# Optimization experiments

Measured on AMD Instinct MI355X. Metric: run time of the kernel, lower is better.

Reference implementation:

```python
import jax, jax.numpy as jnp
import numpy as np

B, L, H, NH = 2, 2048, 1024, 16
HD = H // NH  # head dim = 64


def setup_inputs() -> dict:
    key = jax.random.key(0)
    ks = jax.random.split(key, 8)
    s = 0.02  # small init scale for weights
    return {
        "q": jax.random.normal(ks[0], (B, L, H), jnp.float32),
        "k": jax.random.normal(ks[1], (B, L, H), jnp.float32),
        "v": jax.random.normal(ks[2], (B, L, H), jnp.float32),
        "attention_mask": jnp.zeros((B, NH, L, L), jnp.float32),
        "Wq": jax.random.normal(ks[3], (H, H), jnp.float32) * s,
        "bq": jnp.zeros((H,), jnp.float32),
        "Wk": jax.random.normal(ks[4], (H, H), jnp.float32) * s,
        "bk": jnp.zeros((H,), jnp.float32),
        "Wv": jax.random.normal(ks[5], (H, H), jnp.float32) * s,
        "bv": jnp.zeros((H,), jnp.float32),
        "Wo": jax.random.normal(ks[6], (H, H), jnp.float32) * s,
        "bo": jnp.zeros((H,), jnp.float32),
    }


def reference(q, k, v, attention_mask, Wq, bq, Wk, bk, Wv, bv, Wo, bo):
    # Conv1D (GPT-2 style) projections: x @ W + b
    query = q @ Wq + bq  # [B, L, H]
    key = k @ Wk + bk
    value = v @ Wv + bv
    # split heads -> [B, NH, L, HD]
    qh = query.reshape(B, L, NH, HD).transpose(0, 2, 1, 3)
    kh = key.reshape(B, L, NH, HD).transpose(0, 2, 1, 3)
    vh = value.reshape(B, L, NH, HD).transpose(0, 2, 1, 3)
    # scores: [B, NH, L, L]
    w = jnp.einsum("bhqd,bhkd->bhqk", qh, kh) / jnp.sqrt(jnp.float32(HD))
    w = w + attention_mask
    w = jax.nn.softmax(w, axis=-1)  # dropout p=0 -> identity
    out = jnp.einsum("bhqk,bhkd->bhqd", w, vh)  # [B, NH, L, HD]
    # merge heads -> [B, L, H]
    out = out.transpose(0, 2, 1, 3).reshape(B, L, H)
    return out @ Wo + bo
```

## Files before the change

kernel.cpp:

```cpp
#include <hip/hip_runtime.h>

#define NBATCH 2
#define LSEQ   2048
#define NH     16
#define HD     64
#define HDIM   1024
#define MTOK   4096

typedef unsigned short u16;
typedef __attribute__((ext_vector_type(8))) short bf16x8;
typedef __attribute__((ext_vector_type(4))) float f32x4;

__device__ __forceinline__ u16 f2bf(float f) {
  union { float f; unsigned int u; } x; x.f = f;
  return (u16)((x.u + 0x7fffu + ((x.u >> 16) & 1u)) >> 16);
}

__device__ __forceinline__ void gload_lds16(const void* g, void* l) {
  __builtin_amdgcn_global_load_lds(
      (const __attribute__((address_space(1))) unsigned int*)g,
      (__attribute__((address_space(3))) unsigned int*)l, 16, 0, 0);
}

__global__ void cvt3_kernel(const float* __restrict__ q, const float* __restrict__ k,
                            const float* __restrict__ v, u16* __restrict__ xq,
                            u16* __restrict__ xk, u16* __restrict__ xv) {
  const float* in;
  u16* out;
  if (blockIdx.z == 0)      { in = q; out = xq; }
  else if (blockIdx.z == 1) { in = k; out = xk; }
  else                      { in = v; out = xv; }
  int i = blockIdx.x * blockDim.x + threadIdx.x;
  float4 t = ((const float4*)in)[i];
  ushort4 o;
  o.x = f2bf(t.x); o.y = f2bf(t.y); o.z = f2bf(t.z); o.w = f2bf(t.w);
  ((ushort4*)out)[i] = o;
}

__global__ void wt4_kernel(const float* __restrict__ W0, const float* __restrict__ W1,
                           const float* __restrict__ W2, const float* __restrict__ W3,
                           u16* __restrict__ T0, u16* __restrict__ T1,
                           u16* __restrict__ T2, u16* __restrict__ T3) {
  const float* W;
  u16* Wt;
  if (blockIdx.z == 0)      { W = W0; Wt = T0; }
  else if (blockIdx.z == 1) { W = W1; Wt = T1; }
  else if (blockIdx.z == 2) { W = W2; Wt = T2; }
  else                      { W = W3; Wt = T3; }
  __shared__ float tile[64][65];
  const int k0 = (blockIdx.x & 15) << 6;
  const int n0 = (blockIdx.x >> 4) << 6;
  const int t = threadIdx.x;
#pragma unroll
  for (int i = 0; i < 4; ++i) {
    int idx = t + i * 256;
    int r = idx >> 4, c = (idx & 15) << 2;
    float4 v = *(const float4*)&W[(size_t)(k0 + r) * HDIM + n0 + c];
    tile[r][c] = v.x; tile[r][c + 1] = v.y; tile[r][c + 2] = v.z; tile[r][c + 3] = v.w;
  }
  __syncthreads();
#pragma unroll
  for (int i = 0; i < 4; ++i) {
    int idx = t + i * 256;
    int r = idx >> 4, c = (idx & 15) << 2;
    ushort4 o;
    o.x = f2bf(tile[c][r]);     o.y = f2bf(tile[c + 1][r]);
    o.z = f2bf(tile[c + 2][r]); o.w = f2bf(tile[c + 3][r]);
    *(ushort4*)&Wt[(size_t)(n0 + r) * HDIM + k0 + c] = o;
  }
}

template <int MODE>
__device__ __forceinline__ void gemm_core(u16* As, u16* Bs,
    const u16* __restrict__ A, const u16* __restrict__ Bt,
    const float* __restrict__ bias, void* __restrict__ Cout) {
  const int tid = threadIdx.x;
  const int lane = tid & 63, wid = tid >> 6;
  const int l15 = lane & 15, g = lane >> 4;
  const int m0 = blockIdx.y * 128, n0 = blockIdx.x * 128;
  const int wr = wid >> 1, wc = wid & 1;
  f32x4 acc[4][4];
#pragma unroll
  for (int i = 0; i < 4; ++i)
#pragma unroll
    for (int j = 0; j < 4; ++j) acc[i][j] = (f32x4){0.f, 0.f, 0.f, 0.f};

  for (int t = 0; t < HDIM / 64; ++t) {
    const int k0 = t * 64;
    __syncthreads();
#pragma unroll
    for (int i = 0; i < 4; ++i) {
      const int row = wid * 32 + i * 8 + (lane >> 3);
      const int colb = (lane & 7) * 16;
      gload_lds16((const char*)(A + (size_t)(m0 + row) * HDIM + k0) + colb,
                  (char*)As + (wid * 32 + i * 8) * 128);
      gload_lds16((const char*)(Bt + (size_t)(n0 + row) * HDIM + k0) + colb,
                  (char*)Bs + (wid * 32 + i * 8) * 128);
    }
    __syncthreads();
#pragma unroll
    for (int ks = 0; ks < 2; ++ks) {
      bf16x8 a[4], b[4];
#pragma unroll
      for (int i = 0; i < 4; ++i) {
        const int row = wr * 64 + i * 16 + l15;
        a[i] = *(const bf16x8*)((const char*)As + row * 128 + ks * 64 + g * 16);
      }
#pragma unroll
      for (int j = 0; j < 4; ++j) {
        const int row = wc * 64 + j * 16 + l15;
        b[j] = *(const bf16x8*)((const char*)Bs + row * 128 + ks * 64 + g * 16);
      }
#pragma unroll
      for (int i = 0; i < 4; ++i)
#pragma unroll
        for (int j = 0; j < 4; ++j)
          acc[i][j] = __builtin_amdgcn_mfma_f32_16x16x32_bf16(a[i], b[j], acc[i][j], 0, 0, 0);
    }
  }
#pragma unroll
  for (int i = 0; i < 4; ++i) {
    const int mrow = m0 + wr * 64 + i * 16 + 4 * g;
#pragma unroll
    for (int j = 0; j < 4; ++j) {
      const int ncol = n0 + wc * 64 + j * 16 + l15;
      const float bb = bias[ncol];
      if (MODE == 3) {
        float* o = (float*)Cout;
#pragma unroll
        for (int r = 0; r < 4; ++r)
          o[(size_t)(mrow + r) * HDIM + ncol] = acc[i][j][r] + bb;
      } else if (MODE == 2) {
        const int bidx = mrow >> 11, l0 = mrow & (LSEQ - 1);
        const int h = ncol >> 6, d = ncol & 63;
        ushort4 o4;
        o4.x = f2bf(acc[i][j][0] + bb); o4.y = f2bf(acc[i][j][1] + bb);
        o4.z = f2bf(acc[i][j][2] + bb); o4.w = f2bf(acc[i][j][3] + bb);
        *(ushort4*)&((u16*)Cout)[(((size_t)bidx * NH + h) * HD + d) * LSEQ + l0] = o4;
      } else {
        const int h = ncol >> 6, d = ncol & 63;
        u16* o = (u16*)Cout;
#pragma unroll
        for (int r = 0; r < 4; ++r) {
          const int m = mrow + r;
          const int bidx = m >> 11, l = m & (LSEQ - 1);
          o[(((size_t)bidx * NH + h) * LSEQ + l) * HD + d] = f2bf(acc[i][j][r] + bb);
        }
      }
    }
  }
}

__global__ __launch_bounds__(256, 2) void proj_gemm_kernel(
    const u16* __restrict__ xq, const u16* __restrict__ xk, const u16* __restrict__ xv,
    const u16* __restrict__ WqT, const u16* __restrict__ WkT, const u16* __restrict__ WvT,
    const float* __restrict__ bq, const float* __restrict__ bk, const float* __restrict__ bv,
    u16* __restrict__ Qh, u16* __restrict__ Kh, u16* __restrict__ Vt) {
  __shared__ u16 As[128 * 64];
  __shared__ u16 Bs[128 * 64];
  if (blockIdx.z == 0)      gemm_core<0>(As, Bs, xq, WqT, bq, Qh);
  else if (blockIdx.z == 1) gemm_core<0>(As, Bs, xk, WkT, bk, Kh);
  else                      gemm_core<2>(As, Bs, xv, WvT, bv, Vt);
}

__global__ __launch_bounds__(256, 2) void out_gemm_kernel(
    const u16* __restrict__ A, const u16* __restrict__ WoT,
    const float* __restrict__ bo, float* __restrict__ out) {
  __shared__ u16 As[128 * 64];
  __shared__ u16 Bs[128 * 64];
  gemm_core<3>(As, Bs, A, WoT, bo, out);
}

__global__ __launch_bounds__(256, 4) void attn_kernel(
    const u16* __restrict__ Qh, const u16* __restrict__ Kh,
    const u16* __restrict__ Vt, const float* __restrict__ mask,
    u16* __restrict__ Out ) {
  __shared__ u16 Ks[2][64 * 64];
  __shared__ u16 Vs[2][64 * 64];
  __shared__ u16 Ps[4][16 * 64];
  const int lane = threadIdx.x & 63, w = threadIdx.x >> 6;
  const int l15 = lane & 15, g = lane >> 4;
  const int bh = blockIdx.y;
  const int q0 = blockIdx.x * 64 + w * 16;
  const int NT = LSEQ / 64;

  bf16x8 aq[2];
  {
    const u16* qbase = Qh + ((size_t)bh * LSEQ + q0 + l15) * HD;
    aq[0] = *(const bf16x8*)(qbase + g * 8);
    aq[1] = *(const bf16x8*)(qbase + 32 + g * 8);
  }
  f32x4 o_acc[4];
#pragma unroll
  for (int db = 0; db < 4; ++db) o_acc[db] = (f32x4){0.f, 0.f, 0.f, 0.f};
  float m_run = -1e30f, l_run = 0.f;

  const size_t kbase = (size_t)bh * LSEQ * HD;
  const size_t vbase = (size_t)bh * HD * LSEQ;
  const int srow = w * 16 + (lane >> 3);
  const int scolb = (lane & 7) * 16;

#define STAGE(buf, tt) do {                                                    \
    const int kv0_ = (tt) * 64;                                                \
    _Pragma("unroll")                                                          \
    for (int i_ = 0; i_ < 2; ++i_) {                                           \
      const int row_ = srow + i_ * 8;                                          \
      const int cb_ = scolb ^ ((row_ & 7) << 4);                               \
      gload_lds16((const char*)(Kh + kbase + (size_t)(kv0_ + row_) * HD) + cb_,\
                  (char*)Ks[buf] + (w * 16 + i_ * 8) * 128);                   \
      gload_lds16((const char*)(Vt + vbase + (size_t)row_ * LSEQ + kv0_) + cb_,\
                  (char*)Vs[buf] + (w * 16 + i_ * 8) * 128);                   \
    }                                                                          \
  } while (0)

  const float* mrow = mask + ((size_t)bh * LSEQ + q0 + l15) * LSEQ;
  f32x4 mv[4];

  STAGE(0, 0);
#pragma unroll
  for (int mb = 0; mb < 4; ++mb)
    mv[mb] = *(const f32x4*)(mrow + mb * 16 + 4 * g);
  __syncthreads();

  int cur = 0;
  u16* pbase = Ps[w];
  const int srcbase = (lane & 48) | ((lane & 48) >> 2);
  const int pswz = (l15 & 7) << 4;

  for (int t = 0; t < NT; ++t) {
    if (t + 1 < NT) STAGE(cur ^ 1, t + 1);

    f32x4 s_acc[4];
#pragma unroll
    for (int mb = 0; mb < 4; ++mb) s_acc[mb] = (f32x4){0.f, 0.f, 0.f, 0.f};
    __builtin_amdgcn_s_setprio(1);
#pragma unroll
    for (int ks = 0; ks < 2; ++ks) {
#pragma unroll
      for (int mb = 0; mb < 4; ++mb) {
        const int row = mb * 16 + l15;
        bf16x8 bk = *(const bf16x8*)((const char*)Ks[cur] + row * 128 +
                                     ((ks * 64 + g * 16) ^ ((row & 7) << 4)));
        s_acc[mb] = __builtin_amdgcn_mfma_f32_16x16x32_bf16(bk, aq[ks], s_acc[mb], 0, 0, 0);
      }
    }
    __builtin_amdgcn_s_setprio(0);

    float p[4][4];
    float tmax = -1e30f;
#pragma unroll
    for (int mb = 0; mb < 4; ++mb)
#pragma unroll
      for (int r = 0; r < 4; ++r) {
        p[mb][r] = s_acc[mb][r] * 0.125f + mv[mb][r];
        tmax = fmaxf(tmax, p[mb][r]);
      }
    tmax = fmaxf(tmax, __shfl_xor(tmax, 16));
    tmax = fmaxf(tmax, __shfl_xor(tmax, 32));
    const float mnew = fmaxf(m_run, tmax);
    const float cf = __expf(m_run - mnew);
    m_run = mnew;
    float psum = 0.f;
#pragma unroll
    for (int mb = 0; mb < 4; ++mb)
#pragma unroll
      for (int r = 0; r < 4; ++r) {
        p[mb][r] = __expf(p[mb][r] - mnew);
        psum += p[mb][r];
      }
    psum += __shfl_xor(psum, 16);
    psum += __shfl_xor(psum, 32);
    l_run = l_run * cf + psum;
    float cfr[4];
#pragma unroll
    for (int r = 0; r < 4; ++r) cfr[r] = __shfl(cf, srcbase + r);
#pragma unroll
    for (int db = 0; db < 4; ++db)
#pragma unroll
      for (int r = 0; r < 4; ++r) o_acc[db][r] *= cfr[r];

#pragma unroll
    for (int mb = 0; mb < 4; ++mb) {
      ushort4 pk;
      pk.x = f2bf(p[mb][0]); pk.y = f2bf(p[mb][1]);
      pk.z = f2bf(p[mb][2]); pk.w = f2bf(p[mb][3]);
      *(ushort4*)((char*)pbase + l15 * 128 + ((mb * 32 + 8 * g) ^ pswz)) = pk;
    }

    {
      const int tn = (t + 1 < NT) ? t + 1 : t;
      const float* mnext = mrow + tn * 64;
#pragma unroll
      for (int mb = 0; mb < 4; ++mb)
        mv[mb] = *(const f32x4*)(mnext + mb * 16 + 4 * g);
    }

    asm volatile("s_waitcnt lgkmcnt(0)" ::: "memory");
    __builtin_amdgcn_sched_barrier(0);

    __builtin_amdgcn_s_setprio(1);
#pragma unroll
    for (int s = 0; s < 2; ++s) {
      bf16x8 pa = *(const bf16x8*)((const char*)pbase + l15 * 128 +
                                   ((s * 64 + 16 * g) ^ pswz));
#pragma unroll
      for (int db = 0; db < 4; ++db) {
        const int row = db * 16 + l15;
        bf16x8 bv = *(const bf16x8*)((const char*)Vs[cur] + row * 128 +
                                     ((s * 64 + 16 * g) ^ ((row & 7) << 4)));
        o_acc[db] = __builtin_amdgcn_mfma_f32_16x16x32_bf16(pa, bv, o_acc[db], 0, 0, 0);
      }
    }
    __builtin_amdgcn_s_setprio(0);
    __syncthreads();
    cur ^= 1;
  }
#undef STAGE

  const int b = bh >> 4, h = bh & 15;
  float lr[4];
#pragma unroll
  for (int r = 0; r < 4; ++r) lr[r] = __shfl(l_run, srcbase + r);
#pragma unroll
  for (int r = 0; r < 4; ++r) {
    const float inv = 1.f / lr[r];
    const int qg = q0 + 4 * g + r;
    u16* orow = Out + ((size_t)(b * LSEQ + qg) * NH + h) * HD;
#pragma unroll
    for (int db = 0; db < 4; ++db)
      orow[db * 16 + l15] = f2bf(o_acc[db][r] * inv);
  }
}

extern "C" void kernel_launch(void* const* d_in, const int* in_sizes, int n_in,
                              void* d_out, int out_size, void* d_ws, size_t ws_size,
                              hipStream_t stream) {
  (void)in_sizes; (void)n_in; (void)out_size; (void)ws_size;
  const float* q    = (const float*)d_in[0];
  const float* k    = (const float*)d_in[1];
  const float* v    = (const float*)d_in[2];
  const float* mask = (const float*)d_in[3];
  const float* Wq   = (const float*)d_in[4];
  const float* bq   = (const float*)d_in[5];
  const float* Wk   = (const float*)d_in[6];
  const float* bk   = (const float*)d_in[7];
  const float* Wv   = (const float*)d_in[8];
  const float* bv   = (const float*)d_in[9];
  const float* Wo   = (const float*)d_in[10];
  const float* bo   = (const float*)d_in[11];
  float* out = (float*)d_out;

  char* ws = (char*)d_ws;
  const size_t XB = (size_t)MTOK * HDIM * 2;
  const size_t WB = (size_t)HDIM * HDIM * 2;
  u16* xq   = (u16*)(ws);
  u16* xk   = (u16*)(ws + XB);
  u16* xv   = (u16*)(ws + 2 * XB);
  u16* WqT  = (u16*)(ws + 3 * XB);
  u16* WkT  = (u16*)(ws + 3 * XB + WB);
  u16* WvT  = (u16*)(ws + 3 * XB + 2 * WB);
  u16* WoT  = (u16*)(ws + 3 * XB + 3 * WB);
  u16* Qh   = (u16*)(ws + 3 * XB + 4 * WB);
  u16* Kh   = (u16*)(ws + 4 * XB + 4 * WB);
  u16* Vt   = (u16*)(ws + 5 * XB + 4 * WB);
  u16* aout = (u16*)(ws + 6 * XB + 4 * WB);

  cvt3_kernel<<<dim3((MTOK * HDIM) / 4 / 256, 1, 3), 256, 0, stream>>>(
      q, k, v, xq, xk, xv);
  wt4_kernel<<<dim3(256, 1, 4), 256, 0, stream>>>(
      Wq, Wk, Wv, Wo, WqT, WkT, WvT, WoT);
  proj_gemm_kernel<<<dim3(HDIM / 128, MTOK / 128, 3), 256, 0, stream>>>(
      xq, xk, xv, WqT, WkT, WvT, bq, bk, bv, Qh, Kh, Vt);
  attn_kernel<<<dim3(LSEQ / 64, NBATCH * NH), 256, 0, stream>>>(Qh, Kh, Vt, mask, aout);
  out_gemm_kernel<<<dim3(HDIM / 128, MTOK / 128), 256, 0, stream>>>(aout, WoT, bo, out);
}
```

Before: 232.8 us.

## Stage mask via LDS, lazy softmax rescale, fuse prep kernels, remap GEMM blocks

The attention kernel now loads the mask tiles asynchronously into double-buffered LDS alongside K/V, replacing per-lane direct global loads. It also skips the online-softmax rescale when the new max exceeds the running max by at most 8, which removes the exp and the o_acc multiplies on most iterations. The two prep kernels are merged into one launch, and the GEMM grids are flattened with an XCD-aware block remap. Occupancy hints change as well: GEMMs go to 3 waves per EU and attention to 2. The extra mask LDS lowers attention occupancy, and the lazy rescale assumes exp values stay within a bounded range.

```diff
diff --git a/kernel.cpp b/kernel.cpp
--- a/kernel.cpp
+++ b/kernel.cpp
@@ -22,41 +22,37 @@
       (__attribute__((address_space(3))) unsigned int*)l, 16, 0, 0);
 }
 
-__global__ void cvt3_kernel(const float* __restrict__ q, const float* __restrict__ k,
-                            const float* __restrict__ v, u16* __restrict__ xq,
-                            u16* __restrict__ xk, u16* __restrict__ xv) {
-  const float* in;
-  u16* out;
-  if (blockIdx.z == 0)      { in = q; out = xq; }
-  else if (blockIdx.z == 1) { in = k; out = xk; }
-  else                      { in = v; out = xv; }
-  int i = blockIdx.x * blockDim.x + threadIdx.x;
-  float4 t = ((const float4*)in)[i];
-  ushort4 o;
-  o.x = f2bf(t.x); o.y = f2bf(t.y); o.z = f2bf(t.z); o.w = f2bf(t.w);
-  ((ushort4*)out)[i] = o;
-}
-
-__global__ void wt4_kernel(const float* __restrict__ W0, const float* __restrict__ W1,
-                           const float* __restrict__ W2, const float* __restrict__ W3,
-                           u16* __restrict__ T0, u16* __restrict__ T1,
-                           u16* __restrict__ T2, u16* __restrict__ T3) {
-  const float* W;
-  u16* Wt;
-  if (blockIdx.z == 0)      { W = W0; Wt = T0; }
-  else if (blockIdx.z == 1) { W = W1; Wt = T1; }
-  else if (blockIdx.z == 2) { W = W2; Wt = T2; }
-  else                      { W = W3; Wt = T3; }
+__global__ void prep_kernel(
+    const float* __restrict__ q, const float* __restrict__ k, const float* __restrict__ v,
+    const float* __restrict__ W0, const float* __restrict__ W1,
+    const float* __restrict__ W2, const float* __restrict__ W3,
+    u16* __restrict__ xq, u16* __restrict__ xk, u16* __restrict__ xv,
+    u16* __restrict__ T0, u16* __restrict__ T1, u16* __restrict__ T2,
+    u16* __restrict__ T3) {
   __shared__ float tile[64][65];
-  const int k0 = (blockIdx.x & 15) << 6;
-  const int n0 = (blockIdx.x >> 4) << 6;
+  if (blockIdx.z < 3) {
+    const float* in = (blockIdx.z == 0) ? q : (blockIdx.z == 1) ? k : v;
+    u16* out = (blockIdx.z == 0) ? xq : (blockIdx.z == 1) ? xk : xv;
+    int i = blockIdx.x * blockDim.x + threadIdx.x;
+    float4 t4 = ((const float4*)in)[i];
+    ushort4 o;
+    o.x = f2bf(t4.x); o.y = f2bf(t4.y); o.z = f2bf(t4.z); o.w = f2bf(t4.w);
+    ((ushort4*)out)[i] = o;
+    return;
+  }
+  if (blockIdx.x >= 1024) return;
+  const int sel = blockIdx.x >> 8, bx = blockIdx.x & 255;
+  const float* W = (sel == 0) ? W0 : (sel == 1) ? W1 : (sel == 2) ? W2 : W3;
+  u16* Wt = (sel == 0) ? T0 : (sel == 1) ? T1 : (sel == 2) ? T2 : T3;
+  const int k0 = (bx & 15) << 6;
+  const int n0 = (bx >> 4) << 6;
   const int t = threadIdx.x;
 #pragma unroll
   for (int i = 0; i < 4; ++i) {
     int idx = t + i * 256;
     int r = idx >> 4, c = (idx & 15) << 2;
-    float4 v = *(const float4*)&W[(size_t)(k0 + r) * HDIM + n0 + c];
-    tile[r][c] = v.x; tile[r][c + 1] = v.y; tile[r][c + 2] = v.z; tile[r][c + 3] = v.w;
+    float4 v4 = *(const float4*)&W[(size_t)(k0 + r) * HDIM + n0 + c];
+    tile[r][c] = v4.x; tile[r][c + 1] = v4.y; tile[r][c + 2] = v4.z; tile[r][c + 3] = v4.w;
   }
   __syncthreads();
 #pragma unroll
@@ -71,13 +67,12 @@
 }
 
 template <int MODE>
-__device__ __forceinline__ void gemm_core(u16* As, u16* Bs,
+__device__ __forceinline__ void gemm_core(u16* As, u16* Bs, int m0, int n0,
     const u16* __restrict__ A, const u16* __restrict__ Bt,
     const float* __restrict__ bias, void* __restrict__ Cout) {
   const int tid = threadIdx.x;
   const int lane = tid & 63, wid = tid >> 6;
   const int l15 = lane & 15, g = lane >> 4;
-  const int m0 = blockIdx.y * 128, n0 = blockIdx.x * 128;
   const int wr = wid >> 1, wc = wid & 1;
   f32x4 acc[4][4];
 #pragma unroll
@@ -151,32 +146,40 @@
   }
 }
 
-__global__ __launch_bounds__(256, 2) void proj_gemm_kernel(
+__global__ __launch_bounds__(256, 3) void proj_gemm_kernel(
     const u16* __restrict__ xq, const u16* __restrict__ xk, const u16* __restrict__ xv,
     const u16* __restrict__ WqT, const u16* __restrict__ WkT, const u16* __restrict__ WvT,
     const float* __restrict__ bq, const float* __restrict__ bk, const float* __restrict__ bv,
     u16* __restrict__ Qh, u16* __restrict__ Kh, u16* __restrict__ Vt) {
   __shared__ u16 As[128 * 64];
   __shared__ u16 Bs[128 * 64];
-  if (blockIdx.z == 0)      gemm_core<0>(As, Bs, xq, WqT, bq, Qh);
-  else if (blockIdx.z == 1) gemm_core<0>(As, Bs, xk, WkT, bk, Kh);
-  else                      gemm_core<2>(As, Bs, xv, WvT, bv, Vt);
-}
-
-__global__ __launch_bounds__(256, 2) void out_gemm_kernel(
+  const int h = blockIdx.x;
+  const int l = (h & 7) * 96 + (h >> 3);
+  const int z = l >> 8, rem = l & 255;
+  const int m0 = (rem >> 3) * 128, n0 = (rem & 7) * 128;
+  if (z == 0)      gemm_core<0>(As, Bs, m0, n0, xq, WqT, bq, Qh);
+  else if (z == 1) gemm_core<0>(As, Bs, m0, n0, xk, WkT, bk, Kh);
+  else             gemm_core<2>(As, Bs, m0, n0, xv, WvT, bv, Vt);
+}
+
+__global__ __launch_bounds__(256, 3) void out_gemm_kernel(
     const u16* __restrict__ A, const u16* __restrict__ WoT,
     const float* __restrict__ bo, float* __restrict__ out) {
   __shared__ u16 As[128 * 64];
   __shared__ u16 Bs[128 * 64];
-  gemm_core<3>(As, Bs, A, WoT, bo, out);
-}
-
-__global__ __launch_bounds__(256, 4) void attn_kernel(
+  const int h = blockIdx.x;
+  const int l = (h & 7) * 32 + (h >> 3);
+  const int m0 = (l >> 3) * 128, n0 = (l & 7) * 128;
+  gemm_core<3>(As, Bs, m0, n0, A, WoT, bo, out);
+}
+
+__global__ __launch_bounds__(256, 2) void attn_kernel(
     const u16* __restrict__ Qh, const u16* __restrict__ Kh,
     const u16* __restrict__ Vt, const float* __restrict__ mask,
     u16* __restrict__ Out ) {
   __shared__ u16 Ks[2][64 * 64];
   __shared__ u16 Vs[2][64 * 64];
+  __shared__ float Msh[2][4][16 * 64];
   __shared__ u16 Ps[4][16 * 64];
   const int lane = threadIdx.x & 63, w = threadIdx.x >> 6;
   const int l15 = lane & 15, g = lane >> 4;
@@ -199,8 +202,10 @@
   const size_t vbase = (size_t)bh * HD * LSEQ;
   const int srow = w * 16 + (lane >> 3);
   const int scolb = (lane & 7) * 16;
-
-#define STAGE(buf, tt) do {                                                    \
+  const int row4 = lane >> 4, s16 = lane & 15;
+  const float* mrow_w = mask + ((size_t)bh * LSEQ + q0) * LSEQ;
+
+#define STAGE_KV(buf, tt) do {                                                 \
     const int kv0_ = (tt) * 64;                                                \
     _Pragma("unroll")                                                          \
     for (int i_ = 0; i_ < 2; ++i_) {                                           \
@@ -213,22 +218,29 @@
     }                                                                          \
   } while (0)
 
-  const float* mrow = mask + ((size_t)bh * LSEQ + q0 + l15) * LSEQ;
-  f32x4 mv[4];
-
-  STAGE(0, 0);
-#pragma unroll
-  for (int mb = 0; mb < 4; ++mb)
-    mv[mb] = *(const f32x4*)(mrow + mb * 16 + 4 * g);
+#define STAGE_MASK(buf, tt) do {                                               \
+    const float* mb_ = mrow_w + (size_t)(tt) * 64;                             \
+    _Pragma("unroll")                                                          \
+    for (int i_ = 0; i_ < 4; ++i_) {                                           \
+      const int row_ = 4 * i_ + row4;                                          \
+      const int ch_ = s16 ^ (row_ & 7);                                        \
+      gload_lds16((const char*)(mb_ + (size_t)row_ * LSEQ) + ch_ * 16,         \
+                  (char*)&Msh[buf][w][0] + i_ * 1024);                         \
+    }                                                                          \
+  } while (0)
+
+  STAGE_KV(0, 0);
+  STAGE_MASK(0, 0);
   __syncthreads();
 
   int cur = 0;
   u16* pbase = Ps[w];
   const int srcbase = (lane & 48) | ((lane & 48) >> 2);
   const int pswz = (l15 & 7) << 4;
+  const int hswz = l15 & 7;
 
   for (int t = 0; t < NT; ++t) {
-    if (t + 1 < NT) STAGE(cur ^ 1, t + 1);
+    if (t + 1 < NT) { STAGE_KV(cur ^ 1, t + 1); STAGE_MASK(cur ^ 1, t + 1); }
 
     f32x4 s_acc[4];
 #pragma unroll
@@ -246,38 +258,47 @@
     }
     __builtin_amdgcn_s_setprio(0);
 
+    const char* msw = (const char*)&Msh[cur][w][0] + l15 * 256;
+    f32x4 mval[4];
+#pragma unroll
+    for (int mb = 0; mb < 4; ++mb)
+      mval[mb] = *(const f32x4*)(msw + (((mb * 4 + g) ^ hswz) << 4));
+
     float p[4][4];
     float tmax = -1e30f;
 #pragma unroll
     for (int mb = 0; mb < 4; ++mb)
 #pragma unroll
       for (int r = 0; r < 4; ++r) {
-        p[mb][r] = s_acc[mb][r] * 0.125f + mv[mb][r];
+        p[mb][r] = s_acc[mb][r] * 0.125f + mval[mb][r];
         tmax = fmaxf(tmax, p[mb][r]);
       }
     tmax = fmaxf(tmax, __shfl_xor(tmax, 16));
     tmax = fmaxf(tmax, __shfl_xor(tmax, 32));
-    const float mnew = fmaxf(m_run, tmax);
-    const float cf = __expf(m_run - mnew);
-    m_run = mnew;
+    if (!__all(tmax - m_run <= 8.f)) {
+      const float mnew = fmaxf(m_run, tmax);
+      const float cf = __expf(m_run - mnew);
+      m_run = mnew;
+      l_run *= cf;
+      float cfr[4];
+#pragma unroll
+      for (int r = 0; r < 4; ++r) cfr[r] = __shfl(cf, srcbase + r);
+#pragma unroll
+      for (int db = 0; db < 4; ++db)
+#pragma unroll
+        for (int r = 0; r < 4; ++r) o_acc[db][r] *= cfr[r];
+    }
     float psum = 0.f;
 #pragma unroll
     for (int mb = 0; mb < 4; ++mb)
 #pragma unroll
       for (int r = 0; r < 4; ++r) {
-        p[mb][r] = __expf(p[mb][r] - mnew);
+        p[mb][r] = __expf(p[mb][r] - m_run);
         psum += p[mb][r];
       }
     psum += __shfl_xor(psum, 16);
     psum += __shfl_xor(psum, 32);
-    l_run = l_run * cf + psum;
-    float cfr[4];
-#pragma unroll
-    for (int r = 0; r < 4; ++r) cfr[r] = __shfl(cf, srcbase + r);
-#pragma unroll
-    for (int db = 0; db < 4; ++db)
-#pragma unroll
-      for (int r = 0; r < 4; ++r) o_acc[db][r] *= cfr[r];
+    l_run += psum;
 
 #pragma unroll
     for (int mb = 0; mb < 4; ++mb) {
@@ -286,15 +307,6 @@
       pk.z = f2bf(p[mb][2]); pk.w = f2bf(p[mb][3]);
       *(ushort4*)((char*)pbase + l15 * 128 + ((mb * 32 + 8 * g) ^ pswz)) = pk;
     }
-
-    {
-      const int tn = (t + 1 < NT) ? t + 1 : t;
-      const float* mnext = mrow + tn * 64;
-#pragma unroll
-      for (int mb = 0; mb < 4; ++mb)
-        mv[mb] = *(const f32x4*)(mnext + mb * 16 + 4 * g);
-    }
-
     asm volatile("s_waitcnt lgkmcnt(0)" ::: "memory");
     __builtin_amdgcn_sched_barrier(0);
 
@@ -315,7 +327,8 @@
     __syncthreads();
     cur ^= 1;
   }
-#undef STAGE
+#undef STAGE_KV
+#undef STAGE_MASK
 
   const int b = bh >> 4, h = bh & 15;
   float lr[4];
@@ -365,12 +378,10 @@
   u16* Vt   = (u16*)(ws + 5 * XB + 4 * WB);
   u16* aout = (u16*)(ws + 6 * XB + 4 * WB);
 
-  cvt3_kernel<<<dim3((MTOK * HDIM) / 4 / 256, 1, 3), 256, 0, stream>>>(
-      q, k, v, xq, xk, xv);
-  wt4_kernel<<<dim3(256, 1, 4), 256, 0, stream>>>(
-      Wq, Wk, Wv, Wo, WqT, WkT, WvT, WoT);
-  proj_gemm_kernel<<<dim3(HDIM / 128, MTOK / 128, 3), 256, 0, stream>>>(
+  prep_kernel<<<dim3((MTOK * HDIM) / 4 / 256, 1, 4), 256, 0, stream>>>(
+      q, k, v, Wq, Wk, Wv, Wo, xq, xk, xv, WqT, WkT, WvT, WoT);
+  proj_gemm_kernel<<<768, 256, 0, stream>>>(
       xq, xk, xv, WqT, WkT, WvT, bq, bk, bv, Qh, Kh, Vt);
   attn_kernel<<<dim3(LSEQ / 64, NBATCH * NH), 256, 0, stream>>>(Qh, Kh, Vt, mask, aout);
-  out_gemm_kernel<<<dim3(HDIM / 128, MTOK / 128), 256, 0, stream>>>(aout, WoT, bo, out);
-}
+  out_gemm_kernel<<<256, 256, 0, stream>>>(aout, WoT, bo, out);
+}
```

After: 235.5 us. Within noise of the previous version (+1.1%).
